# Optimization experiments

Measured on AMD Instinct MI355X. Metric: run time of the kernel, lower is better.

## Reference

```python
import jax, jax.numpy as jnp
import numpy as np

B, SEQ, D, H, L, DFF, K = 2, 2048, 256, 8, 2, 1024, 3
DK = D // H
EPS = 1e-5
DROP_CONNECT = 0.5  # eval mode: weight * (1 - rate)


def _make_pe():
    pos = np.arange(SEQ)[:, None].astype(np.float32)
    div = np.exp(np.arange(0, D, 2).astype(np.float32) * (-np.log(10000.0) / D))
    pe = np.zeros((SEQ, D), np.float32)
    pe[:, 0::2] = np.sin(pos * div)
    pe[:, 1::2] = np.cos(pos * div)
    return jnp.asarray(pe)


def setup_inputs() -> dict:
    key = jax.random.key(0)
    ks = jax.random.split(key, 16)
    s = 0.02
    d = {
        'x': jax.random.normal(ks[0], (B, SEQ, 1), jnp.float32),
        'conv_w': jax.random.normal(ks[1], (D, 1, K), jnp.float32) * s,
        'conv_b': jnp.zeros((D,), jnp.float32),
        'bn_g': jnp.ones((D,), jnp.float32),
        'bn_b': jnp.zeros((D,), jnp.float32),
        'pe': _make_pe(),
        'qW': jax.random.normal(ks[2], (L, D, D), jnp.float32) * s,
        'qb': jnp.zeros((L, D), jnp.float32),
        'kW': jax.random.normal(ks[3], (L, D, D), jnp.float32) * s,
        'kb': jnp.zeros((L, D), jnp.float32),
        'vW': jax.random.normal(ks[4], (L, D, D), jnp.float32) * s,
        'vb': jnp.zeros((L, D), jnp.float32),
        'oW': jax.random.normal(ks[5], (L, D, D), jnp.float32) * s,
        'ob': jnp.zeros((L, D), jnp.float32),
        'scale': jnp.ones((L,), jnp.float32),
        'td': jnp.ones((L, H), jnp.float32),
        'ln1g': jnp.ones((L, D), jnp.float32),
        'ln1b': jnp.zeros((L, D), jnp.float32),
        'f1W': jax.random.normal(ks[6], (L, DFF, D), jnp.float32) * s,
        'f1b': jnp.zeros((L, DFF), jnp.float32),
        'f2W': jax.random.normal(ks[7], (L, D, DFF), jnp.float32) * s,
        'f2b': jnp.zeros((L, D), jnp.float32),
        'ln2g': jnp.ones((L, D), jnp.float32),
        'ln2b': jnp.zeros((L, D), jnp.float32),
        'outW': jax.random.normal(ks[8], (1, D), jnp.float32) * s,
        'outb': jnp.zeros((1,), jnp.float32),
    }
    return d


def _layernorm(z, g, b):
    m = z.mean(-1, keepdims=True)
    v = ((z - m) ** 2).mean(-1, keepdims=True)
    return (z - m) / jnp.sqrt(v + EPS) * g + b


def reference(x, conv_w, conv_b, bn_g, bn_b, pe, qW, qb, kW, kb, vW, vb, oW, ob,
              scale, td, ln1g, ln1b, f1W, f1b, f2W, f2b, ln2g, ln2b, outW, outb):
    # CNN frontend: [B,S,1] -> [B,1,S] -> conv -> BN(eval) -> relu -> [B,S,D]
    h = jnp.transpose(x, (0, 2, 1))
    h = jax.lax.conv_general_dilated(h, conv_w, (1,), 'SAME',
                                     dimension_numbers=('NCH', 'OIH', 'NCH'))
    h = h + conv_b[None, :, None]
    # BatchNorm eval with running_mean=0, running_var=1
    h = h / jnp.sqrt(1.0 + EPS) * bn_g[None, :, None] + bn_b[None, :, None]
    h = jax.nn.relu(h)
    h = jnp.transpose(h, (0, 2, 1)) + pe[None]

    inv_sqrt_dk = 1.0 / np.sqrt(DK).astype(np.float32)
    key_pos = jnp.arange(SEQ, dtype=h.dtype)  # decay depends on key index only

    for l in range(L):
        q = (h @ qW[l].T + qb[l]).reshape(B, SEQ, H, DK).transpose(0, 2, 1, 3)
        k = (h @ kW[l].T + kb[l]).reshape(B, SEQ, H, DK).transpose(0, 2, 1, 3)
        v = (h @ vW[l].T + vb[l]).reshape(B, SEQ, H, DK).transpose(0, 2, 1, 3)
        scores = jnp.einsum('bhqd,bhkd->bhqk', q, k) * (inv_sqrt_dk * scale[l])
        decay = jnp.exp(-td[l][:, None, None] * key_pos[None, None, :])  # [H,1,S]
        scores = scores * decay[None]
        attn = jax.nn.softmax(scores, axis=-1) * jax.nn.sigmoid(scores)
        ctx = jnp.einsum('bhqk,bhkd->bhqd', attn, v)
        ctx = ctx.transpose(0, 2, 1, 3).reshape(B, SEQ, D)
        h = _layernorm(h + (ctx @ oW[l].T + ob[l]), ln1g[l], ln1b[l])
        ff = jax.nn.relu(h @ f1W[l].T + f1b[l]) @ f2W[l].T + f2b[l]
        h = _layernorm(h + ff, ln2g[l], ln2b[l])

    last = h[:, -1, :]
    # DropConnectLinear in eval: weight * (1 - drop_connect_rate)
    return last @ (outW * (1.0 - DROP_CONNECT)).T + outb
```

## Files before the change

kernel.cpp:

```cpp
#include <hip/hip_runtime.h>
#include <math.h>

#define B_    2
#define SEQ_  2048
#define D_    256
#define H_    8
#define DK_   32
#define L_    2
#define DFF_  1024

#define TD_CUT 44.0f

typedef short  bf16x8 __attribute__((ext_vector_type(8)));
typedef float  f32x4  __attribute__((ext_vector_type(4)));

__device__ __forceinline__ int compute_kcut(float tdv) {
    int kcut = SEQ_;
    if (tdv > 1e-9f) {
        float kc = TD_CUT / tdv;
        kcut = (kc >= (float)SEQ_) ? SEQ_ : ((int)kc + 1);
    }
    int kcr = (kcut + 63) & ~63;
    if (kcr > SEQ_) kcr = SEQ_;
    return kcr;
}

__device__ __forceinline__ unsigned short f2bf(float f) {
    unsigned int u = __float_as_uint(f);
    unsigned int r = u + 0x7FFFu + ((u >> 16) & 1u);
    return (unsigned short)(r >> 16);
}
__device__ __forceinline__ float bf2f(unsigned short u) {
    return __uint_as_float(((unsigned int)u) << 16);
}
__device__ __forceinline__ float bflo(unsigned int u) {
    return __uint_as_float(u << 16);
}
__device__ __forceinline__ float bfhi(unsigned int u) {
    return __uint_as_float(u & 0xFFFF0000u);
}

__device__ __forceinline__ void gload_lds16(const unsigned short* g, unsigned short* l) {
    __builtin_amdgcn_global_load_lds(
        (const __attribute__((address_space(1))) unsigned int*)(const unsigned int*)g,
        (__attribute__((address_space(3))) unsigned int*)(unsigned int*)l,
        16, 0, 0);
}

__global__ __launch_bounds__(256) void prep_kernel(
    const float* __restrict__ x, const float* __restrict__ w,
    const float* __restrict__ cb, const float* __restrict__ bg,
    const float* __restrict__ bb, const float* __restrict__ pe,
    float* __restrict__ h, unsigned short* __restrict__ hbf,
    const float* __restrict__ p0, const float* __restrict__ p1,
    const float* __restrict__ p2, const float* __restrict__ p3,
    const float* __restrict__ p4, const float* __restrict__ p5,
    unsigned short* __restrict__ q0, unsigned short* __restrict__ q1,
    unsigned short* __restrict__ q2, unsigned short* __restrict__ q3,
    unsigned short* __restrict__ q4, unsigned short* __restrict__ q5,
    float* __restrict__ hts0, float* __restrict__ hts1)
{
    int bid = blockIdx.x;
    if (bid < 768) {
        int t = bid * 256 + threadIdx.x;
        const float* src; unsigned short* dst; int base;
        if (t < 65536) {
            int a = t >> 14;
            src = a == 0 ? p0 : a == 1 ? p1 : a == 2 ? p2 : p3;
            dst = a == 0 ? q0 : a == 1 ? q1 : a == 2 ? q2 : q3;
            base = (t & 16383) * 8;
        } else {
            int u = t - 65536;
            int a = u >> 16;
            src = a ? p5 : p4;
            dst = a ? q5 : q4;
            base = (u & 65535) * 8;
        }
        float4 v0 = *(const float4*)(src + base);
        float4 v1 = *(const float4*)(src + base + 4);
        bf16x8 o;
        o[0] = (short)f2bf(v0.x); o[1] = (short)f2bf(v0.y);
        o[2] = (short)f2bf(v0.z); o[3] = (short)f2bf(v0.w);
        o[4] = (short)f2bf(v1.x); o[5] = (short)f2bf(v1.y);
        o[6] = (short)f2bf(v1.z); o[7] = (short)f2bf(v1.w);
        *(bf16x8*)(dst + base) = o;
        return;
    }
    int bid2 = bid - 768;
    int b    = bid2 >> 6;
    int tile = bid2 & 63;
    int d    = threadIdx.x;

    hts1[bid2 * 256 + d] = 0.f;

    const float* xp = x + b * SEQ_;
    float w0 = w[d * 3 + 0], w1v = w[d * 3 + 1], w2v = w[d * 3 + 2];
    float gg  = rsqrtf(1.f + 1e-5f) * bg[d];
    float cbd = cb[d], bbd = bb[d];

    int s0 = tile * 32;
    float xm1 = (s0 > 0) ? xp[s0 - 1] : 0.f;
    float x0v = xp[s0];
    float hsum = 0.f;
#pragma unroll 4
    for (int r = 0; r < 32; ++r) {
        int s = s0 + r;
        float xp1 = (s < SEQ_ - 1) ? xp[s + 1] : 0.f;
        float acc = xm1 * w0 + x0v * w1v + xp1 * w2v + cbd;
        acc = acc * gg + bbd;
        acc = fmaxf(acc, 0.f);
        float v = acc + pe[s * D_ + d];
        size_t idx = ((size_t)(b * SEQ_ + s)) * D_ + d;
        h[idx] = v;
        unsigned short ub = f2bf(v);
        hbf[idx] = ub;
        hsum += bf2f(ub);
        xm1 = x0v; x0v = xp1;
    }
    hts0[(b * 64 + tile) * 256 + d] = hsum;
}

__global__ __launch_bounds__(256) void gemm_qkv(
    const unsigned short* __restrict__ A,
    const unsigned short* __restrict__ W0, const unsigned short* __restrict__ W1,
    const unsigned short* __restrict__ W2,
    const float* __restrict__ b0, const float* __restrict__ b1,
    const float* __restrict__ b2,
    unsigned short* __restrict__ O0, unsigned short* __restrict__ O1,
    unsigned short* __restrict__ O2,
    const float* __restrict__ td_l,
    const float* __restrict__ hts_l, float* __restrict__ vts_g,
    int M, int N, int K)
{
    __shared__ unsigned short As[2][2][2048];
    __shared__ unsigned short Bs[2][2][2048];
    __shared__ float hsc[256];

    int z = blockIdx.z;
    int tid  = threadIdx.x;

    if (z == 3) {
        if (blockIdx.x != 0 || blockIdx.y >= 16) return;
        int hh = blockIdx.y & 7;
        int b  = blockIdx.y >> 3;
        int kcr = compute_kcut(td_l[hh]);
        if (kcr >= SEQ_) return;
        int tcut = kcr >> 5;
        const float* hb = hts_l + (size_t)b * 64 * 256 + tid;
        float s = 0.f;
#pragma unroll
        for (int t = 0; t < 64; ++t) {
            float v = hb[t * 256];
            s += (t >= tcut) ? v : 0.f;
        }
        hsc[tid] = s;
        __syncthreads();
        int j = tid >> 3, e = tid & 7;
        const unsigned short* wrow = W2 + (size_t)(hh * 32 + j) * 256 + e * 32;
        float dot = 0.f;
#pragma unroll
        for (int i = 0; i < 4; ++i) {
            bf16x8 w8 = *(const bf16x8*)(wrow + i * 8);
#pragma unroll
            for (int t2 = 0; t2 < 8; ++t2)
                dot += hsc[e * 32 + i * 8 + t2] * bf2f((unsigned short)w8[t2]);
        }
        dot += __shfl_xor(dot, 1);
        dot += __shfl_xor(dot, 2);
        dot += __shfl_xor(dot, 4);
        if (e == 0)
            vts_g[(b * H_ + hh) * 32 + j] = dot + (float)(SEQ_ - kcr) * b2[hh * 32 + j];
        return;
    }

    int bm = blockIdx.y * 64, bn = blockIdx.x * 64;
    if (z > 0) {
        float tdmin = td_l[0];
#pragma unroll
        for (int i = 1; i < H_; ++i) tdmin = fminf(tdmin, td_l[i]);
        if ((bm & (SEQ_ - 1)) >= compute_kcut(tdmin)) return;
    }
    const unsigned short* W = (z == 0) ? W0 : (z == 1) ? W1 : W2;
    const float* bias = (z == 0) ? b0 : (z == 1) ? b1 : b2;
    unsigned short* C = (z == 0) ? O0 : (z == 1) ? O1 : O2;

    int wave = tid >> 6, lane = tid & 63;
    int wm = (wave & 1) * 32, wn = (wave >> 1) * 32;

    int sr  = tid >> 2;
    int scb = (tid & 3) ^ ((sr >> 1) & 3);
    const unsigned short* aG = A + (size_t)(bm + sr) * K + scb * 8;
    const unsigned short* wG = W + (size_t)(bn + sr) * K + scb * 8;

    int fr = lane & 15;
    int kb = lane >> 4;
    int cbo = (kb ^ ((fr >> 1) & 3)) * 8;
    int oA0 = (wm + fr) * 32 + cbo;
    int oA1 = (wm + 16 + fr) * 32 + cbo;
    int oB0 = (wn + fr) * 32 + cbo;
    int oB1 = (wn + 16 + fr) * 32 + cbo;

    f32x4 acc[2][2];
#pragma unroll
    for (int i = 0; i < 2; ++i)
#pragma unroll
        for (int j = 0; j < 2; ++j) acc[i][j] = (f32x4){0.f, 0.f, 0.f, 0.f};

    auto stage = [&](int s, int dd) {
        gload_lds16(aG + s * 64,      &As[dd][0][tid * 8]);
        gload_lds16(aG + s * 64 + 32, &As[dd][1][tid * 8]);
        gload_lds16(wG + s * 64,      &Bs[dd][0][tid * 8]);
        gload_lds16(wG + s * 64 + 32, &Bs[dd][1][tid * 8]);
    };

    int nst = K >> 6;
    stage(0, 0);
    __syncthreads();
    for (int s = 0; s < nst; ++s) {
        int dd = s & 1;
        if (s + 1 < nst) stage(s + 1, dd ^ 1);
#pragma unroll
        for (int kk = 0; kk < 2; ++kk) {
            bf16x8 a0f = *(const bf16x8*)&As[dd][kk][oA0];
            bf16x8 a1f = *(const bf16x8*)&As[dd][kk][oA1];
            bf16x8 b0f = *(const bf16x8*)&Bs[dd][kk][oB0];
            bf16x8 b1f = *(const bf16x8*)&Bs[dd][kk][oB1];
            acc[0][0] = __builtin_amdgcn_mfma_f32_16x16x32_bf16(a0f, b0f, acc[0][0], 0, 0, 0);
            acc[0][1] = __builtin_amdgcn_mfma_f32_16x16x32_bf16(a0f, b1f, acc[0][1], 0, 0, 0);
            acc[1][0] = __builtin_amdgcn_mfma_f32_16x16x32_bf16(a1f, b0f, acc[1][0], 0, 0, 0);
            acc[1][1] = __builtin_amdgcn_mfma_f32_16x16x32_bf16(a1f, b1f, acc[1][1], 0, 0, 0);
        }
        __syncthreads();
    }

    int crow = (lane >> 4) * 4;
    int ccol = lane & 15;
#pragma unroll
    for (int j = 0; j < 2; ++j) {
        float bj = bias[bn + wn + j * 16 + ccol];
#pragma unroll
        for (int i = 0; i < 2; ++i) {
#pragma unroll
            for (int r = 0; r < 4; ++r) {
                float v = acc[i][j][r] + bj;
                C[(size_t)(bm + wm + i * 16 + crow + r) * N + bn + wn + j * 16 + ccol] = f2bf(v);
            }
        }
    }
}

__global__ __launch_bounds__(128) void attn_kernel(
    const unsigned short* __restrict__ q, const unsigned short* __restrict__ k,
    const unsigned short* __restrict__ v, const float* __restrict__ vts_g,
    unsigned short* __restrict__ ctxbf,
    const float* __restrict__ scale_p, const float* __restrict__ td_l)
{
    int b = blockIdx.z, hh = blockIdx.y;
    int tid = threadIdx.x;
    int row = tid >> 2;
    int sp  = tid & 3;
    int qrow = blockIdx.x * 32 + row;

    float sc  = 0.17677669529663687f * scale_p[0];
    float tdv = td_l[hh];
    int kcr = compute_kcut(tdv);
    int ntiles = kcr >> 5;

    __shared__ float kt[32][36];
    __shared__ float vt[32][36];
    __shared__ float vts_s[32];

    if (tid < 32) vts_s[tid] = vts_g[(b * H_ + hh) * 32 + tid];

    const unsigned short* qptr = q + ((size_t)(b * SEQ_ + qrow)) * D_ + hh * DK_;
    float qreg[32];
#pragma unroll
    for (int j = 0; j < 4; ++j) {
        uint4 u = ((const uint4*)qptr)[j];
        qreg[j*8+0] = bflo(u.x); qreg[j*8+1] = bfhi(u.x);
        qreg[j*8+2] = bflo(u.y); qreg[j*8+3] = bfhi(u.y);
        qreg[j*8+4] = bflo(u.z); qreg[j*8+5] = bfhi(u.z);
        qreg[j*8+6] = bflo(u.w); qreg[j*8+7] = bfhi(u.w);
    }

    float O[32];
#pragma unroll
    for (int d = 0; d < 32; ++d) O[d] = 0.f;
    float l = 0.f;

    for (int t = 0; t < ntiles; ++t) {
        int k0 = t * 32;
        if (t > 0) __syncthreads();
        {
            int r = tid >> 2, c8 = (tid & 3) * 8;
            size_t goff = ((size_t)(b * SEQ_ + k0 + r)) * D_ + hh * DK_ + c8;
            uint4 uk = *(const uint4*)(k + goff);
            uint4 uv = *(const uint4*)(v + goff);
            *(float4*)&kt[r][c8]     = make_float4(bflo(uk.x), bfhi(uk.x), bflo(uk.y), bfhi(uk.y));
            *(float4*)&kt[r][c8 + 4] = make_float4(bflo(uk.z), bfhi(uk.z), bflo(uk.w), bfhi(uk.w));
            *(float4*)&vt[r][c8]     = make_float4(bflo(uv.x), bfhi(uv.x), bflo(uv.y), bfhi(uv.y));
            *(float4*)&vt[r][c8 + 4] = make_float4(bflo(uv.z), bfhi(uv.z), bflo(uv.w), bfhi(uv.w));
        }
        __syncthreads();

#pragma unroll
        for (int kk = 0; kk < 8; ++kk) {
            int kl = sp * 8 + kk;
            float acc = 0.f;
#pragma unroll
            for (int d4 = 0; d4 < 8; ++d4) {
                float4 kv = *(const float4*)&kt[kl][d4 * 4];
                acc += qreg[d4*4+0] * kv.x + qreg[d4*4+1] * kv.y
                     + qreg[d4*4+2] * kv.z + qreg[d4*4+3] * kv.w;
            }
            float sv = acc * sc * __expf(-tdv * (float)(k0 + kl));
            float e  = __expf(sv);
            float sg = 1.f / (1.f + __expf(-sv));
            float p  = e * sg;
            l += e;
#pragma unroll
            for (int d4 = 0; d4 < 8; ++d4) {
                float4 vv = *(const float4*)&vt[kl][d4 * 4];
                O[d4*4+0] += p * vv.x; O[d4*4+1] += p * vv.y;
                O[d4*4+2] += p * vv.z; O[d4*4+3] += p * vv.w;
            }
        }
    }

    l += __shfl_xor(l, 1);
    l += __shfl_xor(l, 2);
#pragma unroll
    for (int d = 0; d < 32; ++d) {
        O[d] += __shfl_xor(O[d], 1);
        O[d] += __shfl_xor(O[d], 2);
    }

    if (kcr < SEQ_) {
        l += (float)(SEQ_ - kcr);
#pragma unroll
        for (int d = 0; d < 32; ++d) O[d] += 0.5f * vts_s[d];
    }
    float invL = 1.f / l;

    int g = sp;
    unsigned int packed[4];
#pragma unroll
    for (int dd = 0; dd < 8; dd += 2) {
        int d0 = g * 8 + dd, d1 = d0 + 1;
        packed[dd >> 1] = (unsigned)f2bf(O[d0] * invL)
                        | ((unsigned)f2bf(O[d1] * invL) << 16);
    }
    unsigned short* obf = ctxbf + ((size_t)(b * SEQ_ + qrow)) * D_ + hh * DK_ + g * 8;
    *(uint4*)obf = make_uint4(packed[0], packed[1], packed[2], packed[3]);
}

__global__ __launch_bounds__(256) void oproj_ln1(
    const unsigned short* __restrict__ ctx, const unsigned short* __restrict__ wo,
    const float* __restrict__ ob, const float* __restrict__ resid,
    const float* __restrict__ g1, const float* __restrict__ bt1,
    float* __restrict__ h1out, unsigned short* __restrict__ h1bf)
{
    __shared__ unsigned short As[2][512];
    __shared__ unsigned short Bs[2][8192];
    __shared__ float lsum[4][16], lsq[4][16], mean_s[16], inv_s[16];

    int tid = threadIdx.x;
    int wave = tid >> 6, lane = tid & 63;
    int bm = blockIdx.x * 16;
    int fr = lane & 15, kb = lane >> 4;
    int q = kb, cl = fr;
    int swz = (fr >> 1) & 3;

    const unsigned short* gpB[4];
    int dstB[4];
#pragma unroll
    for (int i = 0; i < 4; ++i) {
        int sB = i * 256 + tid;
        int r = sB >> 2, ck = (sB & 3) ^ ((r >> 1) & 3);
        gpB[i] = wo + (size_t)r * 256 + ck * 8;
        dstB[i] = sB * 8;
    }
    const unsigned short* gpA = nullptr;
    if (tid < 64) {
        int r = tid >> 2, ck = (tid & 3) ^ ((r >> 1) & 3);
        gpA = ctx + (size_t)(bm + r) * 256 + ck * 8;
    }

    int oA = fr * 32 + ((kb ^ swz) * 8);
    int oB[4];
#pragma unroll
    for (int t = 0; t < 4; ++t) {
        int n = wave * 64 + t * 16 + fr;
        oB[t] = n * 32 + ((kb ^ swz) * 8);
    }

    f32x4 acc[4];
#pragma unroll
    for (int j = 0; j < 4; ++j) acc[j] = (f32x4){0.f, 0.f, 0.f, 0.f};

    auto stage = [&](int s, int dd) {
#pragma unroll
        for (int i = 0; i < 4; ++i) gload_lds16(gpB[i] + s * 32, &Bs[dd][dstB[i]]);
        if (tid < 64) gload_lds16(gpA + s * 32, &As[dd][tid * 8]);
    };

    stage(0, 0);
    __syncthreads();
    for (int s = 0; s < 8; ++s) {
        int dd = s & 1;
        if (s + 1 < 8) stage(s + 1, dd ^ 1);
        bf16x8 af = *(const bf16x8*)&As[dd][oA];
#pragma unroll
        for (int j = 0; j < 4; ++j)
            acc[j] = __builtin_amdgcn_mfma_f32_16x16x32_bf16(
                af, *(const bf16x8*)&Bs[dd][oB[j]], acc[j], 0, 0, 0);
        __syncthreads();
    }

    float zsum[4] = {0.f, 0.f, 0.f, 0.f}, zsq[4] = {0.f, 0.f, 0.f, 0.f};
    float zv[4][4];
#pragma unroll
    for (int ct = 0; ct < 4; ++ct) {
        int col = wave * 64 + ct * 16 + cl;
        float bj = ob[col];
#pragma unroll
        for (int r = 0; r < 4; ++r) {
            int row = bm + q * 4 + r;
            float z = acc[ct][r] + bj + resid[(size_t)row * 256 + col];
            zv[ct][r] = z;
            zsum[r] += z;
            zsq[r]  += z * z;
        }
    }
#pragma unroll
    for (int r = 0; r < 4; ++r) {
#pragma unroll
        for (int off = 1; off < 16; off <<= 1) {
            zsum[r] += __shfl_xor(zsum[r], off);
            zsq[r]  += __shfl_xor(zsq[r], off);
        }
    }
    if (cl == 0) {
#pragma unroll
        for (int r = 0; r < 4; ++r) {
            lsum[wave][q * 4 + r] = zsum[r];
            lsq[wave][q * 4 + r]  = zsq[r];
        }
    }
    __syncthreads();
    if (tid < 16) {
        float s  = lsum[0][tid] + lsum[1][tid] + lsum[2][tid] + lsum[3][tid];
        float sq = lsq[0][tid] + lsq[1][tid] + lsq[2][tid] + lsq[3][tid];
        float mean = s * (1.f / 256.f);
        float var  = sq * (1.f / 256.f) - mean * mean;
        mean_s[tid] = mean;
        inv_s[tid]  = rsqrtf(var + 1e-5f);
    }
    __syncthreads();

#pragma unroll
    for (int ct = 0; ct < 4; ++ct) {
        int col = wave * 64 + ct * 16 + cl;
        float gc = g1[col], bc = bt1[col];
#pragma unroll
        for (int r = 0; r < 4; ++r) {
            int lr = q * 4 + r;
            float o = (zv[ct][r] - mean_s[lr]) * inv_s[lr] * gc + bc;
            size_t off = (size_t)(bm + lr) * 256 + col;
            h1out[off] = o;
            h1bf[off]  = f2bf(o);
        }
    }
}

__global__ __launch_bounds__(256) void ffn_fused(
    const unsigned short* __restrict__ h1bf, const unsigned short* __restrict__ w1,
    const float* __restrict__ f1b, const unsigned short* __restrict__ w2,
    float* __restrict__ part)
{
    __shared__ unsigned short As[2][1024];
    __shared__ unsigned short Bs[2][8192];
    __shared__ unsigned short ffs[32 * 264];

    int tid = threadIdx.x;
    int wave = tid >> 6, lane = tid & 63;
    int c = blockIdx.x;
    int bm = blockIdx.y * 32;
    int fr = lane & 15, kb = lane >> 4;
    int q = kb, cl = fr;

    const unsigned short* gB1[4];
    const unsigned short* gB2[4];
    int dstB[4];
#pragma unroll
    for (int i = 0; i < 4; ++i) {
        int sB = i * 256 + tid;
        int r = sB >> 2, ck = (sB & 3) ^ ((r >> 1) & 3);
        gB1[i] = w1 + (size_t)(c * 256 + r) * 256 + ck * 8;
        gB2[i] = w2 + (size_t)r * 1024 + c * 256 + ck * 8;
        dstB[i] = sB * 8;
    }
    const unsigned short* gA = nullptr;
    if (tid < 128) {
        int ar = tid >> 2, ack = (tid & 3) ^ ((ar >> 1) & 3);
        gA = h1bf + (size_t)(bm + ar) * 256 + ack * 8;
    }

    int oA1[2], oB[4];
#pragma unroll
    for (int t = 0; t < 2; ++t) {
        int m = t * 16 + fr;
        oA1[t] = m * 32 + ((kb ^ ((m >> 1) & 3)) * 8);
    }
#pragma unroll
    for (int t = 0; t < 4; ++t) {
        int n = wave * 64 + t * 16 + fr;
        oB[t] = n * 32 + ((kb ^ ((n >> 1) & 3)) * 8);
    }

    auto stage1 = [&](int s, int dd) {
#pragma unroll
        for (int i = 0; i < 4; ++i) gload_lds16(gB1[i] + s * 32, &Bs[dd][dstB[i]]);
        if (tid < 128) gload_lds16(gA + s * 32, &As[dd][tid * 8]);
    };
    auto stage2 = [&](int s, int dd) {
#pragma unroll
        for (int i = 0; i < 4; ++i) gload_lds16(gB2[i] + s * 32, &Bs[dd][dstB[i]]);
    };

    f32x4 a1[2][4];
#pragma unroll
    for (int i = 0; i < 2; ++i)
#pragma unroll
        for (int j = 0; j < 4; ++j) a1[i][j] = (f32x4){0.f, 0.f, 0.f, 0.f};

    stage1(0, 0);
    __syncthreads();
    for (int ks = 0; ks < 8; ++ks) {
        int dd = ks & 1;
        if (ks + 1 < 8) stage1(ks + 1, dd ^ 1);
        bf16x8 af[2], bfv[4];
#pragma unroll
        for (int t = 0; t < 2; ++t) af[t] = *(const bf16x8*)&As[dd][oA1[t]];
#pragma unroll
        for (int t = 0; t < 4; ++t) bfv[t] = *(const bf16x8*)&Bs[dd][oB[t]];
#pragma unroll
        for (int i = 0; i < 2; ++i)
#pragma unroll
            for (int j = 0; j < 4; ++j)
                a1[i][j] = __builtin_amdgcn_mfma_f32_16x16x32_bf16(af[i], bfv[j], a1[i][j], 0, 0, 0);
        __syncthreads();
    }

#pragma unroll
    for (int ct = 0; ct < 4; ++ct) {
        int col = wave * 64 + ct * 16 + cl;
        float bj = f1b[c * 256 + col];
#pragma unroll
        for (int rt = 0; rt < 2; ++rt)
#pragma unroll
            for (int r = 0; r < 4; ++r) {
                float v = fmaxf(a1[rt][ct][r] + bj, 0.f);
                ffs[(rt * 16 + q * 4 + r) * 264 + col] = f2bf(v);
            }
    }

    f32x4 a2[2][4];
#pragma unroll
    for (int i = 0; i < 2; ++i)
#pragma unroll
        for (int j = 0; j < 4; ++j) a2[i][j] = (f32x4){0.f, 0.f, 0.f, 0.f};

    stage2(0, 0);
    __syncthreads();
    for (int ks = 0; ks < 8; ++ks) {
        int dd = ks & 1;
        if (ks + 1 < 8) stage2(ks + 1, dd ^ 1);
        bf16x8 af[2], bfv[4];
#pragma unroll
        for (int t = 0; t < 2; ++t)
            af[t] = *(const bf16x8*)&ffs[(t * 16 + fr) * 264 + ks * 32 + kb * 8];
#pragma unroll
        for (int t = 0; t < 4; ++t) bfv[t] = *(const bf16x8*)&Bs[dd][oB[t]];
#pragma unroll
        for (int i = 0; i < 2; ++i)
#pragma unroll
            for (int j = 0; j < 4; ++j)
                a2[i][j] = __builtin_amdgcn_mfma_f32_16x16x32_bf16(af[i], bfv[j], a2[i][j], 0, 0, 0);
        __syncthreads();
    }

#pragma unroll
    for (int ct = 0; ct < 4; ++ct) {
        int col = wave * 64 + ct * 16 + cl;
#pragma unroll
        for (int rt = 0; rt < 2; ++rt)
#pragma unroll
            for (int r = 0; r < 4; ++r)
                part[((size_t)c * 4096 + bm + rt * 16 + q * 4 + r) * 256 + col] = a2[rt][ct][r];
    }
}

__global__ __launch_bounds__(256) void merge_ln2(
    const float* __restrict__ h1, const float* __restrict__ part,
    const float* __restrict__ f2b, const float* __restrict__ g2,
    const float* __restrict__ bt2,
    float* __restrict__ hout, unsigned short* __restrict__ hbf,
    const float* __restrict__ outW, const float* __restrict__ outb,
    float* __restrict__ out, int doFinal,
    float* __restrict__ hts1, int doHts)
{
    __shared__ float red[4][256];

    int wrp = threadIdx.x >> 6;
    int row = blockIdx.x * 4 + wrp;
    int lane = threadIdx.x & 63;
    int d = lane * 4;

    float4 z = *(const float4*)(h1 + (size_t)row * 256 + d);
    float4 b4 = *(const float4*)(f2b + d);
    z.x += b4.x; z.y += b4.y; z.z += b4.z; z.w += b4.w;
#pragma unroll
    for (int c = 0; c < 4; ++c) {
        float4 p = *(const float4*)(part + ((size_t)c * 4096 + row) * 256 + d);
        z.x += p.x; z.y += p.y; z.z += p.z; z.w += p.w;
    }

    float s = z.x + z.y + z.z + z.w;
    float ss = z.x * z.x + z.y * z.y + z.z * z.z + z.w * z.w;
#pragma unroll
    for (int off = 1; off < 64; off <<= 1) {
        s += __shfl_xor(s, off);
        ss += __shfl_xor(ss, off);
    }
    float mean = s * (1.f / 256.f);
    float var = ss * (1.f / 256.f) - mean * mean;
    float inv = rsqrtf(var + 1e-5f);

    float4 g4 = *(const float4*)(g2 + d);
    float4 t4 = *(const float4*)(bt2 + d);
    float4 o;
    o.x = (z.x - mean) * inv * g4.x + t4.x;
    o.y = (z.y - mean) * inv * g4.y + t4.y;
    o.z = (z.z - mean) * inv * g4.z + t4.z;
    o.w = (z.w - mean) * inv * g4.w + t4.w;
    *(float4*)(hout + (size_t)row * 256 + d) = o;
    unsigned short s0 = f2bf(o.x), s1 = f2bf(o.y), s2 = f2bf(o.z), s3 = f2bf(o.w);
    unsigned int u01 = (unsigned)s0 | ((unsigned)s1 << 16);
    unsigned int u23 = (unsigned)s2 | ((unsigned)s3 << 16);
    *(uint2*)&hbf[(size_t)row * 256 + d] = make_uint2(u01, u23);

    if (doHts) {
        *(float4*)&red[wrp][d] = make_float4(bf2f(s0), bf2f(s1), bf2f(s2), bf2f(s3));
        __syncthreads();
        int cidx = threadIdx.x;
        float cs = red[0][cidx] + red[1][cidx] + red[2][cidx] + red[3][cidx];
        int b = blockIdx.x >> 9;
        int tile = (blockIdx.x >> 3) & 63;
        atomicAdd(&hts1[((b << 6) + tile) * 256 + cidx], cs);
    }

    if (doFinal && (row == 2047 || row == 4095)) {
        float4 w4 = *(const float4*)(outW + d);
        float s2f = o.x * w4.x + o.y * w4.y + o.z * w4.z + o.w * w4.w;
#pragma unroll
        for (int off = 1; off < 64; off <<= 1) s2f += __shfl_xor(s2f, off);
        if (lane == 0) out[row >> 11] = s2f * 0.5f + outb[0];
    }
}

extern "C" void kernel_launch(void* const* d_in, const int* in_sizes, int n_in,
                              void* d_out, int out_size, void* d_ws, size_t ws_size,
                              hipStream_t stream)
{
    (void)in_sizes; (void)n_in; (void)out_size; (void)ws_size;
    const float* x      = (const float*)d_in[0];
    const float* conv_w = (const float*)d_in[1];
    const float* conv_b = (const float*)d_in[2];
    const float* bn_g   = (const float*)d_in[3];
    const float* bn_b   = (const float*)d_in[4];
    const float* pe     = (const float*)d_in[5];
    const float* qW     = (const float*)d_in[6];
    const float* qb     = (const float*)d_in[7];
    const float* kW     = (const float*)d_in[8];
    const float* kb     = (const float*)d_in[9];
    const float* vW     = (const float*)d_in[10];
    const float* vb     = (const float*)d_in[11];
    const float* oW     = (const float*)d_in[12];
    const float* ob     = (const float*)d_in[13];
    const float* scale  = (const float*)d_in[14];
    const float* td     = (const float*)d_in[15];
    const float* ln1g   = (const float*)d_in[16];
    const float* ln1b   = (const float*)d_in[17];
    const float* f1W    = (const float*)d_in[18];
    const float* f1b    = (const float*)d_in[19];
    const float* f2W    = (const float*)d_in[20];
    const float* f2b    = (const float*)d_in[21];
    const float* ln2g   = (const float*)d_in[22];
    const float* ln2b   = (const float*)d_in[23];
    const float* outW   = (const float*)d_in[24];
    const float* outb   = (const float*)d_in[25];
    float* out = (float*)d_out;

    float* ws = (float*)d_ws;
    const size_t MT = (size_t)B_ * SEQ_ * D_;
    const size_t HTS = (size_t)B_ * 64 * 256;
    float* h     = ws;
    float* h1    = ws + MT;
    float* part  = ws + 2 * MT;
    float* hts0  = ws + 6 * MT;
    float* hts1  = hts0 + HTS;
    float* vts_g = hts1 + HTS;
    unsigned short* bfb = (unsigned short*)(vts_g + 512);
    unsigned short* h_bf   = bfb;
    unsigned short* ctx_bf = bfb + MT;
    unsigned short* q_bf   = bfb + 2 * MT;
    unsigned short* k_bf   = bfb + 3 * MT;
    unsigned short* v_bf   = bfb + 4 * MT;
    unsigned short* h1_bf  = bfb + 5 * MT;
    unsigned short* wq_bf  = bfb + 6 * MT;
    unsigned short* wk_bf  = wq_bf + MT / 8;
    unsigned short* wv_bf  = wk_bf + MT / 8;
    unsigned short* wo_bf  = wv_bf + MT / 8;
    unsigned short* wf1_bf = wo_bf + MT / 8;
    unsigned short* wf2_bf = wf1_bf + MT / 2;

    const int Mrows = B_ * SEQ_;

    prep_kernel<<<768 + 128, 256, 0, stream>>>(
        x, conv_w, conv_b, bn_g, bn_b, pe, h, h_bf,
        qW, kW, vW, oW, f1W, f2W,
        wq_bf, wk_bf, wv_bf, wo_bf, wf1_bf, wf2_bf, hts0, hts1);

    for (int l = 0; l < L_; ++l) {
        const unsigned short* wq_l  = wq_bf  + (size_t)l * D_ * D_;
        const unsigned short* wk_l  = wk_bf  + (size_t)l * D_ * D_;
        const unsigned short* wv_l  = wv_bf  + (size_t)l * D_ * D_;
        const unsigned short* wo_l  = wo_bf  + (size_t)l * D_ * D_;
        const unsigned short* wf1_l = wf1_bf + (size_t)l * DFF_ * D_;
        const unsigned short* wf2_l = wf2_bf + (size_t)l * DFF_ * D_;
        const float* hts_l = (l == 0) ? hts0 : hts1;

        gemm_qkv<<<dim3(D_ / 64, Mrows / 64, 4), 256, 0, stream>>>(
            h_bf, wq_l, wk_l, wv_l, qb + l * D_, kb + l * D_, vb + l * D_,
            q_bf, k_bf, v_bf, td + l * H_, hts_l, vts_g, Mrows, D_, D_);

        attn_kernel<<<dim3(SEQ_ / 32, H_, B_), 128, 0, stream>>>(
            q_bf, k_bf, v_bf, vts_g, ctx_bf, scale + l, td + l * H_);

        oproj_ln1<<<Mrows / 16, 256, 0, stream>>>(
            ctx_bf, wo_l, ob + l * D_, h,
            ln1g + l * D_, ln1b + l * D_, h1, h1_bf);

        ffn_fused<<<dim3(4, Mrows / 32), 256, 0, stream>>>(
            h1_bf, wf1_l, f1b + l * DFF_, wf2_l, part);

        merge_ln2<<<Mrows / 4, 256, 0, stream>>>(
            h1, part, f2b + l * D_, ln2g + l * D_, ln2b + l * D_,
            h, h_bf, outW, outb, out, (l == L_ - 1) ? 1 : 0,
            hts1, (l == 0) ? 1 : 0);
    }
}
```

Measured before the change: 207.7 us.

## Rewrite attention kernel to use bf16 MFMA for QK^T and PV

Replaces the scalar fp32 dot-product attention with an MFMA-based version: 64-query blocks of 4 waves compute QK^T scores with 16x16x32 bf16 MFMA, write the probabilities as bf16 to LDS, then compute PV with MFMA against a transposed V tile. K/Q are loaded directly into LDS with gload_lds16 instead of being converted to fp32. The goal is to remove the scalar FMA bottleneck and the bf16-to-fp32 conversion traffic. It adds an extra barrier per tile and rounds the probabilities to bf16, which costs some precision.

```diff
diff --git a/kernel.cpp b/kernel.cpp
--- a/kernel.cpp
+++ b/kernel.cpp
@@ -249,7 +249,7 @@
     }
 }
 
-__global__ __launch_bounds__(128) void attn_kernel(
+__global__ __launch_bounds__(256) void attn_kernel(
     const unsigned short* __restrict__ q, const unsigned short* __restrict__ k,
     const unsigned short* __restrict__ v, const float* __restrict__ vts_g,
     unsigned short* __restrict__ ctxbf,
@@ -257,101 +257,108 @@
 {
     int b = blockIdx.z, hh = blockIdx.y;
     int tid = threadIdx.x;
-    int row = tid >> 2;
-    int sp  = tid & 3;
-    int qrow = blockIdx.x * 32 + row;
+    int wave = tid >> 6, lane = tid & 63;
+    int q0r = blockIdx.x * 64;
 
     float sc  = 0.17677669529663687f * scale_p[0];
     float tdv = td_l[hh];
     int kcr = compute_kcut(tdv);
-    int ntiles = kcr >> 5;
-
-    __shared__ float kt[32][36];
-    __shared__ float vt[32][36];
+    int ntiles = kcr >> 6;
+
+    __shared__ unsigned short qt[64 * 32];
+    __shared__ unsigned short kt[64 * 32];
+    __shared__ unsigned short vtT[32 * 72];
+    __shared__ unsigned short pl[64 * 72];
     __shared__ float vts_s[32];
 
     if (tid < 32) vts_s[tid] = vts_g[(b * H_ + hh) * 32 + tid];
 
-    const unsigned short* qptr = q + ((size_t)(b * SEQ_ + qrow)) * D_ + hh * DK_;
-    float qreg[32];
-#pragma unroll
-    for (int j = 0; j < 4; ++j) {
-        uint4 u = ((const uint4*)qptr)[j];
-        qreg[j*8+0] = bflo(u.x); qreg[j*8+1] = bfhi(u.x);
-        qreg[j*8+2] = bflo(u.y); qreg[j*8+3] = bfhi(u.y);
-        qreg[j*8+4] = bflo(u.z); qreg[j*8+5] = bfhi(u.z);
-        qreg[j*8+6] = bflo(u.w); qreg[j*8+7] = bfhi(u.w);
-    }
-
-    float O[32];
-#pragma unroll
-    for (int d = 0; d < 32; ++d) O[d] = 0.f;
-    float l = 0.f;
+    int srow = tid >> 2, sseg = tid & 3;
+    gload_lds16(q + ((size_t)(b * SEQ_ + q0r + srow)) * D_ + hh * DK_ + sseg * 8,
+                &qt[tid * 8]);
+
+    int fr = lane & 15, kb = lane >> 4;
+    const unsigned short* qfrag = &qt[(wave * 16 + fr) * 32 + kb * 8];
+
+    f32x4 acc_o[2];
+    acc_o[0] = (f32x4){0.f, 0.f, 0.f, 0.f};
+    acc_o[1] = (f32x4){0.f, 0.f, 0.f, 0.f};
+    float lpart[4] = {0.f, 0.f, 0.f, 0.f};
 
     for (int t = 0; t < ntiles; ++t) {
-        int k0 = t * 32;
+        int k0 = t * 64;
         if (t > 0) __syncthreads();
         {
-            int r = tid >> 2, c8 = (tid & 3) * 8;
-            size_t goff = ((size_t)(b * SEQ_ + k0 + r)) * D_ + hh * DK_ + c8;
-            uint4 uk = *(const uint4*)(k + goff);
-            uint4 uv = *(const uint4*)(v + goff);
-            *(float4*)&kt[r][c8]     = make_float4(bflo(uk.x), bfhi(uk.x), bflo(uk.y), bfhi(uk.y));
-            *(float4*)&kt[r][c8 + 4] = make_float4(bflo(uk.z), bfhi(uk.z), bflo(uk.w), bfhi(uk.w));
-            *(float4*)&vt[r][c8]     = make_float4(bflo(uv.x), bfhi(uv.x), bflo(uv.y), bfhi(uv.y));
-            *(float4*)&vt[r][c8 + 4] = make_float4(bflo(uv.z), bfhi(uv.z), bflo(uv.w), bfhi(uv.w));
+            gload_lds16(k + ((size_t)(b * SEQ_ + k0 + srow)) * D_ + hh * DK_ + sseg * 8,
+                        &kt[tid * 8]);
+            const unsigned short* vp =
+                v + ((size_t)(b * SEQ_ + k0 + srow)) * D_ + hh * DK_ + sseg * 8;
+            uint4 uv = *(const uint4*)vp;
+            unsigned short ve[8];
+            ve[0] = (unsigned short)(uv.x); ve[1] = (unsigned short)(uv.x >> 16);
+            ve[2] = (unsigned short)(uv.y); ve[3] = (unsigned short)(uv.y >> 16);
+            ve[4] = (unsigned short)(uv.z); ve[5] = (unsigned short)(uv.z >> 16);
+            ve[6] = (unsigned short)(uv.w); ve[7] = (unsigned short)(uv.w >> 16);
+#pragma unroll
+            for (int e = 0; e < 8; ++e)
+                vtT[(sseg * 8 + e) * 72 + srow] = ve[e];
         }
         __syncthreads();
 
-#pragma unroll
-        for (int kk = 0; kk < 8; ++kk) {
-            int kl = sp * 8 + kk;
-            float acc = 0.f;
-#pragma unroll
-            for (int d4 = 0; d4 < 8; ++d4) {
-                float4 kv = *(const float4*)&kt[kl][d4 * 4];
-                acc += qreg[d4*4+0] * kv.x + qreg[d4*4+1] * kv.y
-                     + qreg[d4*4+2] * kv.z + qreg[d4*4+3] * kv.w;
+        f32x4 acc_s[4];
+        bf16x8 aq = *(const bf16x8*)qfrag;
+#pragma unroll
+        for (int kt_i = 0; kt_i < 4; ++kt_i) {
+            bf16x8 bk = *(const bf16x8*)&kt[(kt_i * 16 + fr) * 32 + kb * 8];
+            acc_s[kt_i] = __builtin_amdgcn_mfma_f32_16x16x32_bf16(
+                aq, bk, (f32x4){0.f, 0.f, 0.f, 0.f}, 0, 0, 0);
+        }
+#pragma unroll
+        for (int kt_i = 0; kt_i < 4; ++kt_i) {
+#pragma unroll
+            for (int r = 0; r < 4; ++r) {
+                int key = k0 + kt_i * 16 + fr;
+                float sv = acc_s[kt_i][r] * sc * __expf(-tdv * (float)key);
+                float e  = __expf(sv);
+                float sg = 1.f / (1.f + __expf(-sv));
+                lpart[r] += e;
+                int qrow = wave * 16 + kb * 4 + r;
+                pl[qrow * 72 + kt_i * 16 + fr] = f2bf(e * sg);
             }
-            float sv = acc * sc * __expf(-tdv * (float)(k0 + kl));
-            float e  = __expf(sv);
-            float sg = 1.f / (1.f + __expf(-sv));
-            float p  = e * sg;
-            l += e;
-#pragma unroll
-            for (int d4 = 0; d4 < 8; ++d4) {
-                float4 vv = *(const float4*)&vt[kl][d4 * 4];
-                O[d4*4+0] += p * vv.x; O[d4*4+1] += p * vv.y;
-                O[d4*4+2] += p * vv.z; O[d4*4+3] += p * vv.w;
+        }
+        __syncthreads();
+
+#pragma unroll
+        for (int ks = 0; ks < 2; ++ks) {
+            bf16x8 pa = *(const bf16x8*)&pl[(wave * 16 + fr) * 72 + ks * 32 + kb * 8];
+#pragma unroll
+            for (int nt = 0; nt < 2; ++nt) {
+                bf16x8 vb8 = *(const bf16x8*)&vtT[(nt * 16 + fr) * 72 + ks * 32 + kb * 8];
+                acc_o[nt] = __builtin_amdgcn_mfma_f32_16x16x32_bf16(pa, vb8, acc_o[nt], 0, 0, 0);
             }
         }
     }
 
-    l += __shfl_xor(l, 1);
-    l += __shfl_xor(l, 2);
-#pragma unroll
-    for (int d = 0; d < 32; ++d) {
-        O[d] += __shfl_xor(O[d], 1);
-        O[d] += __shfl_xor(O[d], 2);
-    }
-
-    if (kcr < SEQ_) {
-        l += (float)(SEQ_ - kcr);
-#pragma unroll
-        for (int d = 0; d < 32; ++d) O[d] += 0.5f * vts_s[d];
-    }
-    float invL = 1.f / l;
-
-    int g = sp;
-    unsigned int packed[4];
-#pragma unroll
-    for (int dd = 0; dd < 8; dd += 2) {
-        int d0 = g * 8 + dd, d1 = d0 + 1;
-        packed[dd >> 1] = (unsigned)f2bf(O[d0] * invL)
-                        | ((unsigned)f2bf(O[d1] * invL) << 16);
-    }
-    unsigned short* obf = ctxbf + ((size_t)(b * SEQ_ + qrow)) * D_ + hh * DK_ + g * 8;
-    *(uint4*)obf = make_uint4(packed[0], packed[1], packed[2], packed[3]);
+#pragma unroll
+    for (int r = 0; r < 4; ++r) {
+        lpart[r] += __shfl_xor(lpart[r], 1);
+        lpart[r] += __shfl_xor(lpart[r], 2);
+        lpart[r] += __shfl_xor(lpart[r], 4);
+        lpart[r] += __shfl_xor(lpart[r], 8);
+    }
+    float taill = (kcr < SEQ_) ? (float)(SEQ_ - kcr) : 0.f;
+
+#pragma unroll
+    for (int nt = 0; nt < 2; ++nt) {
+        float vadd = (kcr < SEQ_) ? 0.5f * vts_s[nt * 16 + fr] : 0.f;
+#pragma unroll
+        for (int r = 0; r < 4; ++r) {
+            float invL = 1.f / (lpart[r] + taill);
+            float o = (acc_o[nt][r] + vadd) * invL;
+            int qrow = q0r + wave * 16 + kb * 4 + r;
+            ctxbf[((size_t)(b * SEQ_ + qrow)) * D_ + hh * DK_ + nt * 16 + fr] = f2bf(o);
+        }
+    }
 }
 
 __global__ __launch_bounds__(256) void oproj_ln1(
@@ -745,7 +752,7 @@
             h_bf, wq_l, wk_l, wv_l, qb + l * D_, kb + l * D_, vb + l * D_,
             q_bf, k_bf, v_bf, td + l * H_, hts_l, vts_g, Mrows, D_, D_);
 
-        attn_kernel<<<dim3(SEQ_ / 32, H_, B_), 128, 0, stream>>>(
+        attn_kernel<<<dim3(SEQ_ / 64, H_, B_), 256, 0, stream>>>(
             q_bf, k_bf, v_bf, vts_g, ctx_bf, scale + l, td + l * H_);
 
         oproj_ln1<<<Mrows / 16, 256, 0, stream>>>(
```

Result: faster. 185.5 us (-10.7%).
